# Performance work log

Hardware: AMD Instinct MI355X
Metric: run time of the kernel (lower is better)

Reference implementation:

```python
import jax, jax.numpy as jnp
import numpy as np

B, V, J = 1024, 6890, 24
P_FEAT = (J - 1) * 9  # 207 pose-blendshape features
SMPL_PARENTS = [-1, 0, 0, 0, 1, 2, 3, 4, 5, 6, 7, 8, 9, 9, 9, 12, 13, 14, 16, 17, 18, 19, 20, 21]


def setup_inputs() -> dict:
    key = jax.random.key(0)
    ks = jax.random.split(key, 7)
    return {
        "betas": jax.random.normal(ks[0], (B, 10), jnp.float32),
        "full_pose": jax.random.normal(ks[1], (B, 72), jnp.float32) * 0.3,
        "v_template": jax.random.normal(ks[2], (1, V, 3), jnp.float32),
        "shapedirs": jax.random.normal(ks[3], (V, 3, 10), jnp.float32) * 0.01,
        "posedirs": jax.random.normal(ks[4], (P_FEAT, V * 3), jnp.float32) * 0.01,
        "J_regressor": jax.nn.softmax(jax.random.normal(ks[5], (J, V), jnp.float32), axis=-1),
        "lbs_weights": jax.nn.softmax(jax.random.normal(ks[6], (V, J), jnp.float32) * 4.0, axis=-1),
        "parents": jnp.array(SMPL_PARENTS, dtype=jnp.int32),
    }


def batch_rodrigues(rot_vecs):
    # rot_vecs: [..., 3] axis-angle -> [..., 3, 3] rotation matrices
    angle = jnp.linalg.norm(rot_vecs + 1e-8, axis=-1, keepdims=True)  # [...,1]
    axis = rot_vecs / angle
    s = jnp.sin(angle)[..., None]
    c = jnp.cos(angle)[..., None]
    kx, ky, kz = axis[..., 0], axis[..., 1], axis[..., 2]
    zeros = jnp.zeros_like(kx)
    K = jnp.stack([zeros, -kz, ky, kz, zeros, -kx, -ky, kx, zeros], axis=-1)
    K = K.reshape(rot_vecs.shape[:-1] + (3, 3))
    eye = jnp.eye(3, dtype=rot_vecs.dtype)
    return eye + s * K + (1.0 - c) * (K @ K)


def reference(betas, full_pose, v_template, shapedirs, posedirs, J_regressor, lbs_weights, parents):
    p = [int(x) for x in np.asarray(jax.device_get(parents))]  # static kinematic tree
    b = betas.shape[0]

    # 1) shape blendshapes: minimal shape
    v_shaped = v_template + jnp.einsum("bl,vkl->bvk", betas, shapedirs)  # [B,V,3]

    # 2) rest joints
    J_rest = jnp.einsum("jv,bvk->bjk", J_regressor, v_shaped)  # [B,J,3]

    # 3) pose rotations + pose blendshapes
    rot_mats = batch_rodrigues(full_pose.reshape(b, J, 3))  # [B,J,3,3]
    eye = jnp.eye(3, dtype=rot_mats.dtype)
    pose_feature = (rot_mats[:, 1:] - eye).reshape(b, P_FEAT)  # [B,207]
    v_posed = v_shaped + (pose_feature @ posedirs).reshape(b, V, 3)

    # 4) kinematic chain (sequential composition over fixed 24 joints)
    rel_joints = J_rest.at[:, 1:].add(-J_rest[:, np.array(p[1:])])  # [B,J,3]
    Tm = jnp.zeros((b, J, 4, 4), dtype=rot_mats.dtype)
    Tm = Tm.at[:, :, :3, :3].set(rot_mats)
    Tm = Tm.at[:, :, :3, 3].set(rel_joints)
    Tm = Tm.at[:, :, 3, 3].set(1.0)
    chain = [Tm[:, 0]]
    for i in range(1, J):
        chain.append(chain[p[i]] @ Tm[:, i])
    transforms = jnp.stack(chain, axis=1)  # [B,J,4,4]

    J_posed = transforms[:, :, :3, 3]  # [B,J,3]

    # relative bone transforms: subtract rotated rest joints from translation
    RJ = jnp.einsum("bjmn,bjn->bjm", transforms[:, :, :3, :3], J_rest)
    A = transforms.at[:, :, :3, 3].add(-RJ)  # [B,J,4,4]

    # 5) linear blend skinning: per-vertex weighted transform then apply
    T = jnp.einsum("vj,bjmn->bvmn", lbs_weights, A)  # [B,V,4,4]
    verts = jnp.einsum("bvmn,bvn->bvm", T[:, :, :3, :3], v_posed) + T[:, :, :3, 3]

    return verts, J_posed, J_rest, A, v_shaped
```

## Files before the change

### kernel.cpp

```cpp
#include <hip/hip_runtime.h>
#include <hip/hip_bf16.h>

#define BDIM 1024
#define VDIM 6890
#define NJ   24
#define NCOL (VDIM*3)
#define KPAD 224
#define NPAD 20736
#define NB   8

#define OUT_VERTS   0
#define OUT_JPOSED  21166080
#define OUT_JREST   21239808
#define OUT_A       21313536
#define OUT_VSHAPED 21706752

#define SCRF_PDT    0
#define SCRF_PF     2322432
#define SCRF_JTJS   2437120

#define WSB_PDT   0u
#define WSB_PF    9289728u
#define WSB_JTJS  (9289728u + 458752u)
#define WS_NEED   (9289728u + 458752u + 3168u)

typedef __hip_bfloat16 bf16;
typedef unsigned short ushort_t;
typedef __attribute__((ext_vector_type(8))) short  short8;
typedef __attribute__((ext_vector_type(4))) float  float4v;

__device__ __forceinline__ bf16  tob(float x) { return __float2bfloat16(x); }

__global__ __launch_bounds__(256) void k_jtjs(const float* __restrict__ jreg,
        const float* __restrict__ vt, const float* __restrict__ sd,
        float* __restrict__ jtjs) {
    int j = blockIdx.x;
    int tid = threadIdx.x;
    float acc[33];
#pragma unroll
    for (int i = 0; i < 33; i++) acc[i] = 0.f;
    for (int v = tid; v < VDIM; v += 256) {
        float r = jreg[j*VDIM + v];
#pragma unroll
        for (int m = 0; m < 3; m++) {
            acc[m] += r * vt[v*3+m];
#pragma unroll
            for (int l = 0; l < 10; l++)
                acc[3 + m*10 + l] += r * sd[(v*3+m)*10 + l];
        }
    }
    __shared__ float red[4][33];
    int lane = tid & 63, wid = tid >> 6;
#pragma unroll
    for (int i = 0; i < 33; i++) {
        float x = acc[i];
        for (int off = 32; off > 0; off >>= 1) x += __shfl_down(x, off);
        if (lane == 0) red[wid][i] = x;
    }
    __syncthreads();
    if (tid < 33)
        jtjs[j*33 + tid] = red[0][tid] + red[1][tid] + red[2][tid] + red[3][tid];
}

__global__ __launch_bounds__(256) void k_transpose(const float* __restrict__ pd,
        bf16* __restrict__ pdt) {
    __shared__ bf16 tile[32][65];
    int nt = blockIdx.x * 64;
    int kt = blockIdx.y * 32;
    int t = threadIdx.x;
    for (int i = t; i < 32*64; i += 256) {
        int kk = i >> 6, nn = i & 63;
        int k = kt + kk, n = nt + nn;
        float v = 0.f;
        if (k < 207 && n < NCOL) v = pd[k*NCOL + n];
        tile[kk][nn] = tob(v);
    }
    __syncthreads();
    for (int i = t; i < 32*64; i += 256) {
        int kk = i & 31, nn = i >> 5;
        pdt[(nt + nn)*KPAD + kt + kk] = tile[kk][nn];
    }
}

__global__ __launch_bounds__(64) void k_pose(const float* __restrict__ betas,
        const float* __restrict__ pose, const int* __restrict__ parents,
        const float* __restrict__ jtjs, float* __restrict__ out,
        bf16* __restrict__ wspf) {
    int b = blockIdx.x, t = threadIdx.x;
    __shared__ float R[24][9];
    __shared__ float jrest[24][3];
    __shared__ float rel[24][3];
    __shared__ float ch[24][12];
    __shared__ int par[24];
    if (t < 24) {
        par[t] = parents[t];
        float rx = pose[b*72 + t*3 + 0];
        float ry = pose[b*72 + t*3 + 1];
        float rz = pose[b*72 + t*3 + 2];
        float ax = rx + 1e-8f, ay = ry + 1e-8f, az = rz + 1e-8f;
        float angle = sqrtf(ax*ax + ay*ay + az*az);
        float inv = 1.0f / angle;
        float kx = rx*inv, ky = ry*inv, kz = rz*inv;
        float s = sinf(angle), c = cosf(angle);
        float t1 = 1.0f - c;
        float q = kx*kx + ky*ky + kz*kz;
        R[t][0] = 1.f + t1*(kx*kx - q);
        R[t][1] = -s*kz + t1*kx*ky;
        R[t][2] =  s*ky + t1*kx*kz;
        R[t][3] =  s*kz + t1*kx*ky;
        R[t][4] = 1.f + t1*(ky*ky - q);
        R[t][5] = -s*kx + t1*ky*kz;
        R[t][6] = -s*ky + t1*kx*kz;
        R[t][7] =  s*kx + t1*ky*kz;
        R[t][8] = 1.f + t1*(kz*kz - q);
    }
    __syncthreads();
    for (int i = t; i < KPAD; i += 64) {
        float pf = 0.f;
        if (i < 207) {
            int j = i/9 + 1, e = i - (j-1)*9;
            pf = R[j][e] - ((e == 0 || e == 4 || e == 8) ? 1.f : 0.f);
        }
        wspf[b*KPAD + i] = tob(pf);
    }
    for (int i = t; i < 72; i += 64) {
        int j = i/3, k = i - j*3;
        const float* JJ = &jtjs[j*33];
        float s = JJ[k];
#pragma unroll
        for (int l = 0; l < 10; l++) s += JJ[3 + k*10 + l] * betas[b*10 + l];
        jrest[j][k] = s;
        out[OUT_JREST + b*72 + i] = s;
    }
    __syncthreads();
    for (int i = t; i < 72; i += 64) {
        int j = i/3, k = i - j*3;
        rel[j][k] = jrest[j][k] - (j > 0 ? jrest[par[j]][k] : 0.f);
    }
    __syncthreads();
    if (t < 12) {
        int m = t >> 2, n = t & 3;
        ch[0][t] = (n < 3) ? R[0][m*3+n] : rel[0][m];
    }
    __syncthreads();
    for (int i = 1; i < 24; i++) {
        float val = 0.f;
        if (t < 12) {
            int m = t >> 2, n = t & 3;
            int p = par[i];
            if (n < 3)
                val = ch[p][m*4+0]*R[i][n] + ch[p][m*4+1]*R[i][3+n] + ch[p][m*4+2]*R[i][6+n];
            else
                val = ch[p][m*4+0]*rel[i][0] + ch[p][m*4+1]*rel[i][1]
                    + ch[p][m*4+2]*rel[i][2] + ch[p][m*4+3];
        }
        if (t < 12) ch[i][t] = val;
        __syncthreads();
    }
    for (int i = t; i < 72; i += 64) {
        int j = i/3, k = i - j*3;
        out[OUT_JPOSED + b*72 + i] = ch[j][k*4+3];
    }
    for (int i = t; i < 384; i += 64) {
        int j = i >> 4, e = i & 15, m = e >> 2, n = e & 3;
        float v;
        if (m < 3) {
            if (n < 3) v = ch[j][m*4+n];
            else v = ch[j][m*4+3] - (ch[j][m*4+0]*jrest[j][0] + ch[j][m*4+1]*jrest[j][1]
                                   + ch[j][m*4+2]*jrest[j][2]);
        } else v = (n == 3) ? 1.f : 0.f;
        out[OUT_A + b*384 + i] = v;
    }
}

__global__ __launch_bounds__(256) void k_gemmlbs(const bf16* __restrict__ wspf,
        const bf16* __restrict__ wspdt, const float* __restrict__ betas,
        const float* __restrict__ sd, const float* __restrict__ vt,
        const float* __restrict__ lbs, const float* __restrict__ Amat,
        float* __restrict__ out) {
    __shared__ float dtile[32][196];
    const ushort_t* pf  = (const ushort_t*)wspf;
    const ushort_t* pdt = (const ushort_t*)wspdt;
    int tid  = threadIdx.x;
    int lane = tid & 63, wave = tid >> 6;
    int l15 = lane & 15, quad = lane >> 4;
    int m0 = blockIdx.y * 32;
    int v0 = blockIdx.x * 64;
    int cb = wave * 48;
    int colb = v0*3 + cb;

    float4v acc[2][3] = {};
    for (int c = 0; c < 7; c++) {
        short8 a[2], bb[3];
#pragma unroll
        for (int mf = 0; mf < 2; mf++)
            a[mf] = *reinterpret_cast<const short8*>(pf + (m0 + mf*16 + l15)*KPAD + c*32 + quad*8);
#pragma unroll
        for (int nf = 0; nf < 3; nf++)
            bb[nf] = *reinterpret_cast<const short8*>(pdt + (colb + nf*16 + l15)*KPAD + c*32 + quad*8);
#pragma unroll
        for (int mf = 0; mf < 2; mf++)
#pragma unroll
            for (int nf = 0; nf < 3; nf++)
                acc[mf][nf] = __builtin_amdgcn_mfma_f32_16x16x32_bf16(a[mf], bb[nf], acc[mf][nf], 0, 0, 0);
    }
#pragma unroll
    for (int mf = 0; mf < 2; mf++)
#pragma unroll
        for (int nf = 0; nf < 3; nf++)
#pragma unroll
            for (int r = 0; r < 4; r++)
                dtile[mf*16 + quad*4 + r][cb + nf*16 + l15] = acc[mf][nf][r];
    __syncthreads();

    int v = v0 + lane;
    if (v >= VDIM) return;

    float w[24];
    {
        const float4v* W4 = reinterpret_cast<const float4v*>(lbs + v*24);
#pragma unroll
        for (int q = 0; q < 6; q++) {
            float4v x = W4[q];
#pragma unroll
            for (int e = 0; e < 4; e++) w[q*4+e] = x[e];
        }
    }
    float vtv[3];
#pragma unroll
    for (int m = 0; m < 3; m++) vtv[m] = vt[v*3 + m];
    float sdv[30];
#pragma unroll
    for (int i = 0; i < 30; i++) sdv[i] = sd[v*30 + i];

    int wv = __builtin_amdgcn_readfirstlane(wave);
    float* vsh = out + OUT_VSHAPED;

#pragma unroll 1
    for (int bb2 = 0; bb2 < 8; bb2++) {
        int b  = m0 + wv*8 + bb2;
        int bl = wv*8 + bb2;
        const float* __restrict__ Ab = Amat + (size_t)b*384;

        float T[12];
#pragma unroll
        for (int e = 0; e < 12; e++) T[e] = 0.f;
#pragma unroll
        for (int j = 0; j < 24; j++) {
#pragma unroll
            for (int e = 0; e < 12; e++)
                T[e] = fmaf(w[j], Ab[j*16 + e], T[e]);
        }

        float vs[3];
#pragma unroll
        for (int m = 0; m < 3; m++) {
            float s = vtv[m];
#pragma unroll
            for (int l = 0; l < 10; l++) s += betas[b*10 + l] * sdv[m*10 + l];
            vs[m] = s;
        }

        float vp0 = vs[0] + dtile[bl][lane*3 + 0];
        float vp1 = vs[1] + dtile[bl][lane*3 + 1];
        float vp2 = vs[2] + dtile[bl][lane*3 + 2];
        int base = b*NCOL + v*3;
#pragma unroll
        for (int m = 0; m < 3; m++) {
            float o = T[m*4+3] + T[m*4]*vp0 + T[m*4+1]*vp1 + T[m*4+2]*vp2;
            out[base + m]  = o;
            vsh[base + m]  = vs[m];
        }
    }
}

__global__ __launch_bounds__(256) void k_posegemm(const bf16* __restrict__ wspf,
        const bf16* __restrict__ wspdt, float* __restrict__ dout) {
    const ushort_t* pf  = (const ushort_t*)wspf;
    const ushort_t* pdt = (const ushort_t*)wspdt;
    int lane = threadIdx.x & 63;
    int wave = threadIdx.x >> 6;
    int l15 = lane & 15, quad = lane >> 4;
    int m0 = blockIdx.y * 32;
    int n0 = blockIdx.x * 256 + wave * 64;
    float4v acc[2][4] = {};
    for (int c = 0; c < 7; c++) {
        short8 a[2], bb[4];
#pragma unroll
        for (int mf = 0; mf < 2; mf++)
            a[mf] = *reinterpret_cast<const short8*>(pf + (m0 + mf*16 + l15)*KPAD + c*32 + quad*8);
#pragma unroll
        for (int nf = 0; nf < 4; nf++)
            bb[nf] = *reinterpret_cast<const short8*>(pdt + (n0 + nf*16 + l15)*KPAD + c*32 + quad*8);
#pragma unroll
        for (int mf = 0; mf < 2; mf++)
#pragma unroll
            for (int nf = 0; nf < 4; nf++)
                acc[mf][nf] = __builtin_amdgcn_mfma_f32_16x16x32_bf16(a[mf], bb[nf], acc[mf][nf], 0, 0, 0);
    }
#pragma unroll
    for (int mf = 0; mf < 2; mf++)
#pragma unroll
        for (int nf = 0; nf < 4; nf++) {
            int col = n0 + nf*16 + l15;
            if (col < NCOL) {
#pragma unroll
                for (int r = 0; r < 4; r++) {
                    int row = m0 + mf*16 + quad*4 + r;
                    dout[row*NCOL + col] = acc[mf][nf][r];
                }
            }
        }
}

__global__ __launch_bounds__(256) void k_lbs(const float* __restrict__ betas,
        const float* __restrict__ sd, const float* __restrict__ vt,
        const float* __restrict__ lbs, const float* __restrict__ Amat,
        float* __restrict__ out) {
    int tid = threadIdx.x;
    int v = blockIdx.x*256 + tid;
    if (v >= VDIM) return;
    int b0 = blockIdx.y * NB;
    float w[24];
    {
        const float4v* W4 = reinterpret_cast<const float4v*>(lbs + v*24);
#pragma unroll
        for (int q = 0; q < 6; q++) {
            float4v x = W4[q];
#pragma unroll
            for (int e = 0; e < 4; e++) w[q*4+e] = x[e];
        }
    }
    float vtv[3];
#pragma unroll
    for (int m = 0; m < 3; m++) vtv[m] = vt[v*3 + m];
    float sdv[30];
#pragma unroll
    for (int i = 0; i < 30; i++) sdv[i] = sd[v*30 + i];
    float* vsh = out + OUT_VSHAPED;
#pragma unroll 1
    for (int bb = 0; bb < NB; bb++) {
        int b = b0 + bb;
        const float* __restrict__ Ab = Amat + (size_t)b*384;
        float T[12];
#pragma unroll
        for (int e = 0; e < 12; e++) T[e] = 0.f;
#pragma unroll
        for (int j = 0; j < 24; j++) {
#pragma unroll
            for (int e = 0; e < 12; e++)
                T[e] = fmaf(w[j], Ab[j*16 + e], T[e]);
        }
        float vs[3];
#pragma unroll
        for (int m = 0; m < 3; m++) {
            float s = vtv[m];
#pragma unroll
            for (int l = 0; l < 10; l++) s += betas[b*10 + l] * sdv[m*10 + l];
            vs[m] = s;
        }
        int base = b*NCOL + v*3;
        float vp0 = vs[0] + vsh[base + 0];
        float vp1 = vs[1] + vsh[base + 1];
        float vp2 = vs[2] + vsh[base + 2];
#pragma unroll
        for (int m = 0; m < 3; m++) {
            float o = T[m*4+3] + T[m*4]*vp0 + T[m*4+1]*vp1 + T[m*4+2]*vp2;
            out[base + m] = o;
            vsh[base + m] = vs[m];
        }
    }
}

extern "C" void kernel_launch(void* const* d_in, const int* in_sizes, int n_in,
                              void* d_out, int out_size, void* d_ws, size_t ws_size,
                              hipStream_t stream) {
    const float *betas = nullptr, *pose = nullptr, *vt = nullptr, *sd = nullptr,
                *pd = nullptr, *jreg = nullptr, *lbs = nullptr;
    const int* parents = nullptr;
    for (int i = 0; i < n_in; i++) {
        switch (in_sizes[i]) {
            case 10240:   betas = (const float*)d_in[i]; break;
            case 73728:   pose  = (const float*)d_in[i]; break;
            case 20670:   vt    = (const float*)d_in[i]; break;
            case 206700:  sd    = (const float*)d_in[i]; break;
            case 4278690: pd    = (const float*)d_in[i]; break;
            case 24:      parents = (const int*)d_in[i]; break;
            case 165360:
                if (!jreg) jreg = (const float*)d_in[i];
                else       lbs  = (const float*)d_in[i];
                break;
            default: break;
        }
    }
    float* out = (float*)d_out;
    if (d_ws && ws_size >= (size_t)WS_NEED) {
        bf16*  ws_pdt  = (bf16*)((char*)d_ws + WSB_PDT);
        bf16*  ws_pf   = (bf16*)((char*)d_ws + WSB_PF);
        float* ws_jtjs = (float*)((char*)d_ws + WSB_JTJS);
        k_jtjs<<<24, 256, 0, stream>>>(jreg, vt, sd, ws_jtjs);
        k_transpose<<<dim3(324, 7), 256, 0, stream>>>(pd, ws_pdt);
        k_pose<<<BDIM, 64, 0, stream>>>(betas, pose, parents, ws_jtjs, out, ws_pf);
        k_gemmlbs<<<dim3(108, 32), 256, 0, stream>>>(ws_pf, ws_pdt, betas, sd, vt, lbs,
                                                     out + OUT_A, out);
    } else {
        bf16*  ws_pdt  = (bf16*)(out + SCRF_PDT);
        bf16*  ws_pf   = (bf16*)(out + SCRF_PF);
        float* ws_jtjs = out + SCRF_JTJS;
        k_jtjs<<<24, 256, 0, stream>>>(jreg, vt, sd, ws_jtjs);
        k_transpose<<<dim3(324, 7), 256, 0, stream>>>(pd, ws_pdt);
        k_pose<<<BDIM, 64, 0, stream>>>(betas, pose, parents, ws_jtjs, out, ws_pf);
        k_posegemm<<<dim3(81, 32), 256, 0, stream>>>(ws_pf, ws_pdt, out + OUT_VSHAPED);
        k_lbs<<<dim3(27, BDIM/NB), 256, 0, stream>>>(betas, sd, vt, lbs, out + OUT_A, out);
    }
}
```

Baseline: 342.0 us.

## Compute LBS transform blend with split-bf16 MFMA instead of scalar FMAs

Replaces the per-vertex scalar 24x12 weighted-transform loop with MFMA matrix multiplies. LBS weights are pre-split into hi/lo bf16 parts by a new packing kernel, and the A matrices are split on the fly, with three MFMAs per tile to approach fp32 accuracy. The shaped-vertex plus pose-offset sum is staged in shared memory first, and outputs are written per quad lane. This adds an extra kernel launch, extra workspace and a second barrier, and it slightly changes numerics compared with the fp32 version.

```diff
diff --git a/kernel.cpp b/kernel.cpp
--- a/kernel.cpp
+++ b/kernel.cpp
@@ -8,6 +8,7 @@
 #define KPAD 224
 #define NPAD 20736
 #define NB   8
+#define VPAD 6912
 
 #define OUT_VERTS   0
 #define OUT_JPOSED  21166080
@@ -21,8 +22,10 @@
 
 #define WSB_PDT   0u
 #define WSB_PF    9289728u
-#define WSB_JTJS  (9289728u + 458752u)
-#define WS_NEED   (9289728u + 458752u + 3168u)
+#define WSB_JTJS  9748480u
+#define WSB_WHI   9752064u
+#define WSB_WLO   10194432u
+#define WS_NEED   10636800u
 
 typedef __hip_bfloat16 bf16;
 typedef unsigned short ushort_t;
@@ -30,6 +33,16 @@
 typedef __attribute__((ext_vector_type(4))) float  float4v;
 
 __device__ __forceinline__ bf16  tob(float x) { return __float2bfloat16(x); }
+
+__device__ __forceinline__ ushort_t bf16_rne(float x) {
+    unsigned u = __builtin_bit_cast(unsigned, x);
+    unsigned r = (u + 0x7FFFu + ((u >> 16) & 1u)) >> 16;
+    return (ushort_t)r;
+}
+__device__ __forceinline__ float bf16_to_f(ushort_t h) {
+    unsigned u = ((unsigned)h) << 16;
+    return __builtin_bit_cast(float, u);
+}
 
 __global__ __launch_bounds__(256) void k_jtjs(const float* __restrict__ jreg,
         const float* __restrict__ vt, const float* __restrict__ sd,
@@ -80,6 +93,17 @@
         int kk = i & 31, nn = i >> 5;
         pdt[(nt + nn)*KPAD + kt + kk] = tile[kk][nn];
     }
+}
+
+__global__ __launch_bounds__(256) void k_wpack(const float* __restrict__ lbs,
+        ushort_t* __restrict__ whi, ushort_t* __restrict__ wlo) {
+    int idx = blockIdx.x*256 + threadIdx.x;
+    if (idx >= VPAD*32) return;
+    int v = idx >> 5, j = idx & 31;
+    float x = (v < VDIM && j < 24) ? lbs[v*24 + j] : 0.f;
+    ushort_t h = bf16_rne(x);
+    whi[idx] = h;
+    wlo[idx] = bf16_rne(x - bf16_to_f(h));
 }
 
 __global__ __launch_bounds__(64) void k_pose(const float* __restrict__ betas,
@@ -176,8 +200,8 @@
 __global__ __launch_bounds__(256) void k_gemmlbs(const bf16* __restrict__ wspf,
         const bf16* __restrict__ wspdt, const float* __restrict__ betas,
         const float* __restrict__ sd, const float* __restrict__ vt,
-        const float* __restrict__ lbs, const float* __restrict__ Amat,
-        float* __restrict__ out) {
+        const ushort_t* __restrict__ whi, const ushort_t* __restrict__ wlo,
+        const float* __restrict__ Amat, float* __restrict__ out) {
     __shared__ float dtile[32][196];
     const ushort_t* pf  = (const ushort_t*)wspf;
     const ushort_t* pdt = (const ushort_t*)wspdt;
@@ -189,87 +213,102 @@
     int cb = wave * 48;
     int colb = v0*3 + cb;
 
-    float4v acc[2][3] = {};
-    for (int c = 0; c < 7; c++) {
-        short8 a[2], bb[3];
+    {
+        float4v acc[2][3] = {};
+        for (int c = 0; c < 7; c++) {
+            short8 a[2], bb[3];
+#pragma unroll
+            for (int mf = 0; mf < 2; mf++)
+                a[mf] = *reinterpret_cast<const short8*>(pf + (m0 + mf*16 + l15)*KPAD + c*32 + quad*8);
+#pragma unroll
+            for (int nf = 0; nf < 3; nf++)
+                bb[nf] = *reinterpret_cast<const short8*>(pdt + (colb + nf*16 + l15)*KPAD + c*32 + quad*8);
+#pragma unroll
+            for (int mf = 0; mf < 2; mf++)
+#pragma unroll
+                for (int nf = 0; nf < 3; nf++)
+                    acc[mf][nf] = __builtin_amdgcn_mfma_f32_16x16x32_bf16(a[mf], bb[nf], acc[mf][nf], 0, 0, 0);
+        }
 #pragma unroll
         for (int mf = 0; mf < 2; mf++)
-            a[mf] = *reinterpret_cast<const short8*>(pf + (m0 + mf*16 + l15)*KPAD + c*32 + quad*8);
-#pragma unroll
-        for (int nf = 0; nf < 3; nf++)
-            bb[nf] = *reinterpret_cast<const short8*>(pdt + (colb + nf*16 + l15)*KPAD + c*32 + quad*8);
-#pragma unroll
-        for (int mf = 0; mf < 2; mf++)
 #pragma unroll
             for (int nf = 0; nf < 3; nf++)
-                acc[mf][nf] = __builtin_amdgcn_mfma_f32_16x16x32_bf16(a[mf], bb[nf], acc[mf][nf], 0, 0, 0);
-    }
-#pragma unroll
-    for (int mf = 0; mf < 2; mf++)
-#pragma unroll
-        for (int nf = 0; nf < 3; nf++)
-#pragma unroll
-            for (int r = 0; r < 4; r++)
-                dtile[mf*16 + quad*4 + r][cb + nf*16 + l15] = acc[mf][nf][r];
-    __syncthreads();
-
+#pragma unroll
+                for (int r = 0; r < 4; r++)
+                    dtile[mf*16 + quad*4 + r][cb + nf*16 + l15] = acc[mf][nf][r];
+    }
+    __syncthreads();
+
+    int wv = __builtin_amdgcn_readfirstlane(wave);
     int v = v0 + lane;
-    if (v >= VDIM) return;
-
-    float w[24];
-    {
-        const float4v* W4 = reinterpret_cast<const float4v*>(lbs + v*24);
-#pragma unroll
-        for (int q = 0; q < 6; q++) {
-            float4v x = W4[q];
-#pragma unroll
-            for (int e = 0; e < 4; e++) w[q*4+e] = x[e];
-        }
-    }
-    float vtv[3];
-#pragma unroll
-    for (int m = 0; m < 3; m++) vtv[m] = vt[v*3 + m];
-    float sdv[30];
-#pragma unroll
-    for (int i = 0; i < 30; i++) sdv[i] = sd[v*30 + i];
-
-    int wv = __builtin_amdgcn_readfirstlane(wave);
     float* vsh = out + OUT_VSHAPED;
-
+    if (v < VDIM) {
+        float vtv[3];
+#pragma unroll
+        for (int m = 0; m < 3; m++) vtv[m] = vt[v*3 + m];
+        float sdv[30];
+#pragma unroll
+        for (int i = 0; i < 30; i++) sdv[i] = sd[v*30 + i];
+#pragma unroll 1
+        for (int bb2 = 0; bb2 < 8; bb2++) {
+            int b  = m0 + wv*8 + bb2;
+            int bl = wv*8 + bb2;
+            float vs[3];
+#pragma unroll
+            for (int m = 0; m < 3; m++) {
+                float s = vtv[m];
+#pragma unroll
+                for (int l = 0; l < 10; l++) s += betas[b*10 + l] * sdv[m*10 + l];
+                vs[m] = s;
+            }
+            int base = b*NCOL + v*3;
+#pragma unroll
+            for (int n = 0; n < 3; n++) {
+                float d = dtile[bl][lane*3 + n];
+                dtile[bl][lane*3 + n] = vs[n] + d;
+                vsh[base + n] = vs[n];
+            }
+        }
+    }
+    __syncthreads();
+
+    short8 bhi[4], blo[4];
+#pragma unroll
+    for (int nf = 0; nf < 4; nf++) {
+        int vv = v0 + nf*16 + l15;
+        bhi[nf] = *reinterpret_cast<const short8*>(whi + vv*32 + quad*8);
+        blo[nf] = *reinterpret_cast<const short8*>(wlo + vv*32 + quad*8);
+    }
+    bool aval = (quad < 3) && (l15 < 12);
 #pragma unroll 1
     for (int bb2 = 0; bb2 < 8; bb2++) {
         int b  = m0 + wv*8 + bb2;
         int bl = wv*8 + bb2;
-        const float* __restrict__ Ab = Amat + (size_t)b*384;
-
-        float T[12];
-#pragma unroll
-        for (int e = 0; e < 12; e++) T[e] = 0.f;
-#pragma unroll
-        for (int j = 0; j < 24; j++) {
-#pragma unroll
-            for (int e = 0; e < 12; e++)
-                T[e] = fmaf(w[j], Ab[j*16 + e], T[e]);
-        }
-
-        float vs[3];
-#pragma unroll
-        for (int m = 0; m < 3; m++) {
-            float s = vtv[m];
-#pragma unroll
-            for (int l = 0; l < 10; l++) s += betas[b*10 + l] * sdv[m*10 + l];
-            vs[m] = s;
-        }
-
-        float vp0 = vs[0] + dtile[bl][lane*3 + 0];
-        float vp1 = vs[1] + dtile[bl][lane*3 + 1];
-        float vp2 = vs[2] + dtile[bl][lane*3 + 2];
-        int base = b*NCOL + v*3;
-#pragma unroll
-        for (int m = 0; m < 3; m++) {
-            float o = T[m*4+3] + T[m*4]*vp0 + T[m*4+1]*vp1 + T[m*4+2]*vp2;
-            out[base + m]  = o;
-            vsh[base + m]  = vs[m];
+        float af[8];
+#pragma unroll
+        for (int i = 0; i < 8; i++)
+            af[i] = aval ? Amat[(size_t)b*384 + (quad*8 + i)*16 + l15] : 0.f;
+        short8 ahi, alo;
+#pragma unroll
+        for (int i = 0; i < 8; i++) {
+            ushort_t h = bf16_rne(af[i]);
+            ahi[i] = (short)h;
+            alo[i] = (short)bf16_rne(af[i] - bf16_to_f(h));
+        }
+#pragma unroll
+        for (int nf = 0; nf < 4; nf++) {
+            float4v acc = {};
+            acc = __builtin_amdgcn_mfma_f32_16x16x32_bf16(ahi, bhi[nf], acc, 0, 0, 0);
+            acc = __builtin_amdgcn_mfma_f32_16x16x32_bf16(alo, bhi[nf], acc, 0, 0, 0);
+            acc = __builtin_amdgcn_mfma_f32_16x16x32_bf16(ahi, blo[nf], acc, 0, 0, 0);
+            int vl = nf*16 + l15;
+            float vp0 = dtile[bl][vl*3 + 0];
+            float vp1 = dtile[bl][vl*3 + 1];
+            float vp2 = dtile[bl][vl*3 + 2];
+            if (quad < 3 && v0 + vl < VDIM) {
+                float o = acc[3] + acc[0]*vp0 + acc[1]*vp1 + acc[2]*vp2;
+                out[(size_t)b*NCOL + (v0 + vl)*3 + quad] = o;
+            }
         }
     }
 }
@@ -395,14 +434,17 @@
     }
     float* out = (float*)d_out;
     if (d_ws && ws_size >= (size_t)WS_NEED) {
-        bf16*  ws_pdt  = (bf16*)((char*)d_ws + WSB_PDT);
-        bf16*  ws_pf   = (bf16*)((char*)d_ws + WSB_PF);
-        float* ws_jtjs = (float*)((char*)d_ws + WSB_JTJS);
+        bf16*     ws_pdt  = (bf16*)((char*)d_ws + WSB_PDT);
+        bf16*     ws_pf   = (bf16*)((char*)d_ws + WSB_PF);
+        float*    ws_jtjs = (float*)((char*)d_ws + WSB_JTJS);
+        ushort_t* ws_whi  = (ushort_t*)((char*)d_ws + WSB_WHI);
+        ushort_t* ws_wlo  = (ushort_t*)((char*)d_ws + WSB_WLO);
         k_jtjs<<<24, 256, 0, stream>>>(jreg, vt, sd, ws_jtjs);
         k_transpose<<<dim3(324, 7), 256, 0, stream>>>(pd, ws_pdt);
+        k_wpack<<<(VPAD*32 + 255)/256, 256, 0, stream>>>(lbs, ws_whi, ws_wlo);
         k_pose<<<BDIM, 64, 0, stream>>>(betas, pose, parents, ws_jtjs, out, ws_pf);
-        k_gemmlbs<<<dim3(108, 32), 256, 0, stream>>>(ws_pf, ws_pdt, betas, sd, vt, lbs,
-                                                     out + OUT_A, out);
+        k_gemmlbs<<<dim3(108, 32), 256, 0, stream>>>(ws_pf, ws_pdt, betas, sd, vt,
+                                                     ws_whi, ws_wlo, out + OUT_A, out);
     } else {
         bf16*  ws_pdt  = (bf16*)(out + SCRF_PDT);
         bf16*  ws_pf   = (bf16*)(out + SCRF_PF);
```

Measured after the change: 300.2 us. 12.2% less time.
